# Performance work log

Measured on AMD Instinct MI355X. Metric: run time of the kernel, lower is better.

## Reference

```python
import jax, jax.numpy as jnp
import numpy as np

MAX_CAV = 5


def setup_inputs() -> dict:
    key = jax.random.key(0)
    k1, k2, k3, k4, k5 = jax.random.split(key, 5)
    # ragged group lengths, each <= MAX_CAV, sum = 25
    record_len = jnp.array([3, 5, 2, 4, 1, 5, 3, 2], dtype=jnp.int32)
    N, C, H, W = 25, 256, 48, 176
    x = jax.random.normal(k1, (N, C, H, W), dtype=jnp.float32)
    W1 = jax.random.normal(k2, (MAX_CAV, 2 * MAX_CAV), dtype=jnp.float32) * 0.3
    W2 = jax.random.normal(k3, (MAX_CAV, MAX_CAV), dtype=jnp.float32) * 0.3
    conv_w = jax.random.normal(k4, (MAX_CAV,), dtype=jnp.float32) * 0.3
    conv_b = jax.random.normal(k5, (1,), dtype=jnp.float32) * 0.1
    return dict(x=x, record_len=record_len, W1=W1, W2=W2, conv_w=conv_w, conv_b=conv_b)


def _pad_regroup(x, record_len, max_cav):
    # scatter ragged tokens into a zero-padded [bs, max_cav, C, H, W] buffer
    N = x.shape[0]
    bs = record_len.shape[0]
    cum = jnp.cumsum(record_len)
    tok = jnp.arange(N)
    b = jnp.searchsorted(cum, tok, side='right')      # batch id per token
    slot = tok - (cum[b] - record_len[b])             # position within group
    padded = jnp.zeros((bs, max_cav) + x.shape[1:], x.dtype)
    return padded.at[b, slot].set(x)


def reference(x, record_len, W1, W2, conv_w, conv_b):
    padded = _pad_regroup(x, record_len, MAX_CAV)     # [bs, M, C, H, W]
    # AdaptiveAvg/MaxPool3d(1) over (C,H,W); padded slots are all-zero -> max=0
    x_avg = padded.mean(axis=(2, 3, 4))               # [bs, M]
    x_max = padded.max(axis=(2, 3, 4))                # [bs, M]
    x_sq = jnp.concatenate([x_avg, x_max], axis=1)    # [bs, 2M]
    gate = jax.nn.relu(jax.nn.sigmoid(x_sq @ W1.T) @ W2.T)  # [bs, M]
    scaled = padded * gate[:, :, None, None, None]
    # 1x1x1 Conv3d(M -> 1) == weighted sum over CAV axis + bias, then ReLU
    out = jax.nn.relu(jnp.einsum('m,bmchw->bchw', conv_w, scaled) + conv_b[0])
    return out
```

## Files before the change

### kernel.cpp

```cpp
#include <hip/hip_runtime.h>
#include <hip/hip_bf16.h>
#include <math.h>

#define CHW      2162688
#define V4       540672
#define BPT      64
#define V4_BLK   8448
#define ITERS    33
#define MAXCAV   5

typedef float f32x4 __attribute__((ext_vector_type(4)));

__global__ __launch_bounds__(256) void k_reduce(const float4* __restrict__ x,
                                                float* __restrict__ psum,
                                                float* __restrict__ pmax) {
    const int t   = blockIdx.y;
    const int blk = blockIdx.x;
    const long base = (long)t * V4 + (long)blk * V4_BLK;

    float s = 0.0f;
    float mx = -INFINITY;
    #pragma unroll 4
    for (int i = 0; i < ITERS; ++i) {
        float4 v = x[base + i * 256 + threadIdx.x];
        s += (v.x + v.y) + (v.z + v.w);
        mx = fmaxf(mx, fmaxf(fmaxf(v.x, v.y), fmaxf(v.z, v.w)));
    }

    __shared__ float ssum[256];
    __shared__ float smax[256];
    ssum[threadIdx.x] = s;
    smax[threadIdx.x] = mx;
    __syncthreads();
    #pragma unroll
    for (int off = 128; off > 0; off >>= 1) {
        if (threadIdx.x < off) {
            ssum[threadIdx.x] += ssum[threadIdx.x + off];
            smax[threadIdx.x] = fmaxf(smax[threadIdx.x], smax[threadIdx.x + off]);
        }
        __syncthreads();
    }
    if (threadIdx.x == 0) {
        psum[t * BPT + blk] = ssum[0];
        pmax[t * BPT + blk] = smax[0];
    }
}

__global__ __launch_bounds__(256) void k_gate(const float* __restrict__ psum,
                                              const float* __restrict__ pmax,
                                              const int*   __restrict__ record_len,
                                              const float* __restrict__ W1,
                                              const float* __restrict__ W2,
                                              const float* __restrict__ conv_w,
                                              int*   __restrict__ starts,
                                              float* __restrict__ coefs,
                                              int bs, int ntok) {
    __shared__ float tsum[32];
    __shared__ float tmax[32];
    const int wave = threadIdx.x >> 6;
    const int lane = threadIdx.x & 63;

    for (int t = wave; t < ntok; t += 4) {
        float s = psum[t * BPT + lane];
        float m = pmax[t * BPT + lane];
        #pragma unroll
        for (int off = 32; off > 0; off >>= 1) {
            s += __shfl_xor(s, off, 64);
            m = fmaxf(m, __shfl_xor(m, off, 64));
        }
        if (lane == 0) { tsum[t] = s; tmax[t] = m; }
    }
    __syncthreads();

    if ((int)threadIdx.x < bs) {
        const int b = threadIdx.x;
        int start = 0;
        for (int i = 0; i < b; ++i) start += record_len[i];
        const int len = record_len[b];

        float xsq[2 * MAXCAV];
        #pragma unroll
        for (int m = 0; m < MAXCAV; ++m) {
            const bool valid = m < len;
            xsq[m]          = valid ? tsum[start + m] * (1.0f / (float)CHW) : 0.0f;
            xsq[MAXCAV + m] = valid ? tmax[start + m] : 0.0f;
        }
        float h[MAXCAV];
        #pragma unroll
        for (int j = 0; j < MAXCAV; ++j) {
            float a = 0.0f;
            #pragma unroll
            for (int k = 0; k < 2 * MAXCAV; ++k) a += xsq[k] * W1[j * 2 * MAXCAV + k];
            h[j] = 1.0f / (1.0f + expf(-a));
        }
        starts[b] = start;
        #pragma unroll
        for (int m = 0; m < MAXCAV; ++m) {
            float g = 0.0f;
            #pragma unroll
            for (int j = 0; j < MAXCAV; ++j) g += h[j] * W2[m * MAXCAV + j];
            g = fmaxf(g, 0.0f);
            coefs[b * MAXCAV + m] = conv_w[m] * g;
        }
    }
}

template <int LEN>
__device__ __forceinline__ void apply_one(const float4* __restrict__ x,
                                          const float* __restrict__ c,
                                          float bias, int start,
                                          long obase, int idx,
                                          float4* __restrict__ out) {
    float ax = bias, ay = bias, az = bias, aw = bias;
    #pragma unroll
    for (int m = 0; m < LEN; ++m) {
        float4 v = x[(long)(start + m) * V4 + idx];
        ax += c[m] * v.x;
        ay += c[m] * v.y;
        az += c[m] * v.z;
        aw += c[m] * v.w;
    }
    f32x4 acc;
    acc.x = fmaxf(ax, 0.0f);
    acc.y = fmaxf(ay, 0.0f);
    acc.z = fmaxf(az, 0.0f);
    acc.w = fmaxf(aw, 0.0f);
    __builtin_nontemporal_store(acc, (f32x4*)(out + obase + idx));
}

template <int LEN>
__device__ __forceinline__ void apply_pair(const float4* __restrict__ x,
                                           const float* __restrict__ c,
                                           float bias, int start,
                                           long obase, int idx0,
                                           float4* __restrict__ out) {
    apply_one<LEN>(x, c, bias, start, obase, idx0, out);
    apply_one<LEN>(x, c, bias, start, obase, idx0 + 256, out);
}

__global__ __launch_bounds__(256) void k_apply(const float4* __restrict__ x,
                                               const int*   __restrict__ record_len,
                                               const int*   __restrict__ starts,
                                               const float* __restrict__ coefs,
                                               const float* __restrict__ conv_b,
                                               float4* __restrict__ out,
                                               int bs) {
    const int idx0 = blockIdx.x * 512 + threadIdx.x;
    const float bias = conv_b[0];

    for (int b = 0; b < bs; ++b) {
        const int len   = record_len[b];
        const int start = starts[b];
        float c[MAXCAV];
        #pragma unroll
        for (int m = 0; m < MAXCAV; ++m) c[m] = coefs[b * MAXCAV + m];
        const long obase = (long)b * V4;

        switch (len) {
            case 1:  apply_pair<1>(x, c, bias, start, obase, idx0, out); break;
            case 2:  apply_pair<2>(x, c, bias, start, obase, idx0, out); break;
            case 3:  apply_pair<3>(x, c, bias, start, obase, idx0, out); break;
            case 4:  apply_pair<4>(x, c, bias, start, obase, idx0, out); break;
            default: apply_pair<5>(x, c, bias, start, obase, idx0, out); break;
        }
    }
}

extern "C" void kernel_launch(void* const* d_in, const int* in_sizes, int n_in,
                              void* d_out, int out_size, void* d_ws, size_t ws_size,
                              hipStream_t stream) {
    const float* x  = (const float*)d_in[0];
    const int*   rl = (const int*)d_in[1];
    const float* W1 = (const float*)d_in[2];
    const float* W2 = (const float*)d_in[3];
    const float* cw = (const float*)d_in[4];
    const float* cb = (const float*)d_in[5];
    float4* out = (float4*)d_out;

    char* ws = (char*)d_ws;
    float* psum   = (float*)(ws);
    float* pmax   = (float*)(ws + 6400);
    int*   starts = (int*)  (ws + 12800);
    float* coefs  = (float*)(ws + 12832);

    const int ntok = in_sizes[0] / CHW;
    const int bs   = in_sizes[1];

    k_reduce<<<dim3(BPT, ntok), 256, 0, stream>>>((const float4*)x, psum, pmax);
    k_gate<<<1, 256, 0, stream>>>(psum, pmax, rl, W1, W2, cw, starts, coefs, bs, ntok);
    k_apply<<<V4 / 512, 256, 0, stream>>>((const float4*)x, rl, starts, coefs, cb, out, bs);
}
```

Before: 84.66 us.

## Fuse reduce, gate and apply into one cooperative persistent kernel

Replaces the three-kernel pipeline with a single cooperative kernel of 1024 blocks. Each block first reduces a contiguous chunk of x that may straddle two tokens, then a grid-wide sync follows, every block recomputes the gate coefficients redundantly, and then applies the weighted sum to its slice. This is meant to remove two kernel launch gaps and the serial single-block gate kernel, at the cost of a grid barrier and repeated gate work in every block. It keeps the old three-kernel path as a fallback when occupancy is too low.

```diff
diff --git a/kernel.cpp b/kernel.cpp
--- a/kernel.cpp
+++ b/kernel.cpp
@@ -1,15 +1,186 @@
 #include <hip/hip_runtime.h>
-#include <hip/hip_bf16.h>
+#include <hip/hip_cooperative_groups.h>
 #include <math.h>
 
-#define CHW      2162688
-#define V4       540672
+#define CHW     2162688
+#define V4      540672
+#define NTOK    25
+#define NBLK    1024
+#define CHUNK1  13200
+#define CHUNK3  528
+#define MAXCAV  5
+#define NBATCH  8
+
 #define BPT      64
 #define V4_BLK   8448
 #define ITERS    33
-#define MAXCAV   5
-
+
+namespace cg = cooperative_groups;
 typedef float f32x4 __attribute__((ext_vector_type(4)));
+
+__device__ __forceinline__ void relu_store(float ax, float ay, float az, float aw,
+                                           float4* __restrict__ out, int o) {
+    f32x4 acc;
+    acc.x = fmaxf(ax, 0.0f);
+    acc.y = fmaxf(ay, 0.0f);
+    acc.z = fmaxf(az, 0.0f);
+    acc.w = fmaxf(aw, 0.0f);
+    __builtin_nontemporal_store(acc, (f32x4*)(out + o));
+}
+
+template <int LEN>
+__device__ __forceinline__ void apply_idx(const float4* __restrict__ x,
+                                          const float* c, float bias,
+                                          int start, int obase, int idx,
+                                          float4* __restrict__ out) {
+    float ax = bias, ay = bias, az = bias, aw = bias;
+    #pragma unroll
+    for (int m = 0; m < LEN; ++m) {
+        float4 v = x[(start + m) * V4 + idx];
+        ax += c[m] * v.x;
+        ay += c[m] * v.y;
+        az += c[m] * v.z;
+        aw += c[m] * v.w;
+    }
+    relu_store(ax, ay, az, aw, out, obase + idx);
+}
+
+template <int LEN>
+__device__ __forceinline__ void apply_chunk(const float4* __restrict__ x,
+                                            const float* c, float bias,
+                                            int start, int obase, int base3,
+                                            int tid, float4* __restrict__ out) {
+    apply_idx<LEN>(x, c, bias, start, obase, base3 + tid, out);
+    apply_idx<LEN>(x, c, bias, start, obase, base3 + 256 + tid, out);
+    if (tid < CHUNK3 - 512)
+        apply_idx<LEN>(x, c, bias, start, obase, base3 + 512 + tid, out);
+}
+
+__global__ __launch_bounds__(256, 4) void k_fused(
+    const float4* __restrict__ x,
+    const int*   __restrict__ record_len,
+    const float* __restrict__ W1,
+    const float* __restrict__ W2,
+    const float* __restrict__ conv_w,
+    const float* __restrict__ conv_b,
+    float4* __restrict__ out,
+    float* __restrict__ ps,
+    float* __restrict__ pm)
+{
+    const int tid  = threadIdx.x;
+    const int bid  = blockIdx.x;
+    const int lane = tid & 63;
+    const int wave = tid >> 6;
+
+    const int base  = bid * CHUNK1;
+    const int t0    = base / V4;
+    const int split = min((t0 + 1) * V4 - base, CHUNK1);
+
+    float s0 = 0.f, s1 = 0.f, m0 = -INFINITY, m1 = -INFINITY;
+    #pragma unroll 2
+    for (int li = tid; li < CHUNK1; li += 256) {
+        float4 v = x[base + li];
+        float vs = (v.x + v.y) + (v.z + v.w);
+        float vm = fmaxf(fmaxf(v.x, v.y), fmaxf(v.z, v.w));
+        if (li < split) { s0 += vs; m0 = fmaxf(m0, vm); }
+        else            { s1 += vs; m1 = fmaxf(m1, vm); }
+    }
+    #pragma unroll
+    for (int off = 32; off > 0; off >>= 1) {
+        s0 += __shfl_xor(s0, off, 64);
+        s1 += __shfl_xor(s1, off, 64);
+        m0 = fmaxf(m0, __shfl_xor(m0, off, 64));
+        m1 = fmaxf(m1, __shfl_xor(m1, off, 64));
+    }
+    __shared__ float rs0[4], rs1[4], rm0[4], rm1[4];
+    if (lane == 0) { rs0[wave] = s0; rs1[wave] = s1; rm0[wave] = m0; rm1[wave] = m1; }
+    __syncthreads();
+    if (tid == 0) {
+        ps[2 * bid]     = rs0[0] + rs0[1] + rs0[2] + rs0[3];
+        ps[2 * bid + 1] = rs1[0] + rs1[1] + rs1[2] + rs1[3];
+        pm[2 * bid]     = fmaxf(fmaxf(rm0[0], rm0[1]), fmaxf(rm0[2], rm0[3]));
+        pm[2 * bid + 1] = fmaxf(fmaxf(rm1[0], rm1[1]), fmaxf(rm1[2], rm1[3]));
+    }
+
+    cg::this_grid().sync();
+
+    __shared__ float tsum[NTOK], tmax[NTOK];
+    __shared__ float scoef[NBATCH][MAXCAV];
+    __shared__ int   sstart[NBATCH], slen[NBATCH];
+    __shared__ float sbias;
+
+    for (int t = wave; t < NTOK; t += 4) {
+        const int b_lo = (t == 0) ? 0 : ((t - 1) * V4 + CHUNK1 - 1) / CHUNK1;
+        const int b_hi = min(NBLK - 1, ((t + 1) * V4 + CHUNK1 - 1) / CHUNK1 - 1);
+        float s = 0.f, m = -INFINITY;
+        for (int b = b_lo + lane; b <= b_hi; b += 64) {
+            const int tb = (b * CHUNK1) / V4;
+            if (tb == t)     { s += ps[2 * b];     m = fmaxf(m, pm[2 * b]); }
+            if (tb == t - 1) { s += ps[2 * b + 1]; m = fmaxf(m, pm[2 * b + 1]); }
+        }
+        #pragma unroll
+        for (int off = 32; off > 0; off >>= 1) {
+            s += __shfl_xor(s, off, 64);
+            m = fmaxf(m, __shfl_xor(m, off, 64));
+        }
+        if (lane == 0) { tsum[t] = s; tmax[t] = m; }
+    }
+    __syncthreads();
+
+    if (tid < NBATCH) {
+        const int b = tid;
+        int start = 0;
+        for (int i = 0; i < b; ++i) start += record_len[i];
+        const int len = record_len[b];
+        sstart[b] = start;
+        slen[b]   = len;
+
+        float xsq[2 * MAXCAV];
+        #pragma unroll
+        for (int m = 0; m < MAXCAV; ++m) {
+            const bool valid = m < len;
+            xsq[m]          = valid ? tsum[start + m] * (1.0f / (float)CHW) : 0.0f;
+            xsq[MAXCAV + m] = valid ? tmax[start + m] : 0.0f;
+        }
+        float h[MAXCAV];
+        #pragma unroll
+        for (int j = 0; j < MAXCAV; ++j) {
+            float a = 0.0f;
+            #pragma unroll
+            for (int k = 0; k < 2 * MAXCAV; ++k) a += xsq[k] * W1[j * 2 * MAXCAV + k];
+            h[j] = 1.0f / (1.0f + expf(-a));
+        }
+        #pragma unroll
+        for (int m = 0; m < MAXCAV; ++m) {
+            float g = 0.0f;
+            #pragma unroll
+            for (int j = 0; j < MAXCAV; ++j) g += h[j] * W2[m * MAXCAV + j];
+            scoef[b][m] = conv_w[m] * fmaxf(g, 0.0f);
+        }
+        if (b == 0) sbias = conv_b[0];
+    }
+    __syncthreads();
+
+    const float bias  = sbias;
+    const int   base3 = bid * CHUNK3;
+
+    for (int b = 0; b < NBATCH; ++b) {
+        const int len   = slen[b];
+        const int start = sstart[b];
+        float c[MAXCAV];
+        #pragma unroll
+        for (int m = 0; m < MAXCAV; ++m) c[m] = scoef[b][m];
+        const int obase = b * V4;
+
+        switch (len) {
+            case 1:  apply_chunk<1>(x, c, bias, start, obase, base3, tid, out); break;
+            case 2:  apply_chunk<2>(x, c, bias, start, obase, base3, tid, out); break;
+            case 3:  apply_chunk<3>(x, c, bias, start, obase, base3, tid, out); break;
+            case 4:  apply_chunk<4>(x, c, bias, start, obase, base3, tid, out); break;
+            default: apply_chunk<5>(x, c, bias, start, obase, base3, tid, out); break;
+        }
+    }
+}
 
 __global__ __launch_bounds__(256) void k_reduce(const float4* __restrict__ x,
                                                 float* __restrict__ psum,
@@ -99,43 +270,18 @@
             float g = 0.0f;
             #pragma unroll
             for (int j = 0; j < MAXCAV; ++j) g += h[j] * W2[m * MAXCAV + j];
-            g = fmaxf(g, 0.0f);
-            coefs[b * MAXCAV + m] = conv_w[m] * g;
+            coefs[b * MAXCAV + m] = conv_w[m] * fmaxf(g, 0.0f);
         }
     }
 }
 
 template <int LEN>
-__device__ __forceinline__ void apply_one(const float4* __restrict__ x,
-                                          const float* __restrict__ c,
-                                          float bias, int start,
-                                          long obase, int idx,
-                                          float4* __restrict__ out) {
-    float ax = bias, ay = bias, az = bias, aw = bias;
-    #pragma unroll
-    for (int m = 0; m < LEN; ++m) {
-        float4 v = x[(long)(start + m) * V4 + idx];
-        ax += c[m] * v.x;
-        ay += c[m] * v.y;
-        az += c[m] * v.z;
-        aw += c[m] * v.w;
-    }
-    f32x4 acc;
-    acc.x = fmaxf(ax, 0.0f);
-    acc.y = fmaxf(ay, 0.0f);
-    acc.z = fmaxf(az, 0.0f);
-    acc.w = fmaxf(aw, 0.0f);
-    __builtin_nontemporal_store(acc, (f32x4*)(out + obase + idx));
-}
-
-template <int LEN>
-__device__ __forceinline__ void apply_pair(const float4* __restrict__ x,
-                                           const float* __restrict__ c,
-                                           float bias, int start,
-                                           long obase, int idx0,
-                                           float4* __restrict__ out) {
-    apply_one<LEN>(x, c, bias, start, obase, idx0, out);
-    apply_one<LEN>(x, c, bias, start, obase, idx0 + 256, out);
+__device__ __forceinline__ void fb_pair(const float4* __restrict__ x,
+                                        const float* c, float bias, int start,
+                                        long obase, int idx0,
+                                        float4* __restrict__ out) {
+    apply_idx<LEN>(x, c, bias, start, (int)obase, idx0, out);
+    apply_idx<LEN>(x, c, bias, start, (int)obase, idx0 + 256, out);
 }
 
 __global__ __launch_bounds__(256) void k_apply(const float4* __restrict__ x,
@@ -157,11 +303,11 @@
         const long obase = (long)b * V4;
 
         switch (len) {
-            case 1:  apply_pair<1>(x, c, bias, start, obase, idx0, out); break;
-            case 2:  apply_pair<2>(x, c, bias, start, obase, idx0, out); break;
-            case 3:  apply_pair<3>(x, c, bias, start, obase, idx0, out); break;
-            case 4:  apply_pair<4>(x, c, bias, start, obase, idx0, out); break;
-            default: apply_pair<5>(x, c, bias, start, obase, idx0, out); break;
+            case 1:  fb_pair<1>(x, c, bias, start, obase, idx0, out); break;
+            case 2:  fb_pair<2>(x, c, bias, start, obase, idx0, out); break;
+            case 3:  fb_pair<3>(x, c, bias, start, obase, idx0, out); break;
+            case 4:  fb_pair<4>(x, c, bias, start, obase, idx0, out); break;
+            default: fb_pair<5>(x, c, bias, start, obase, idx0, out); break;
         }
     }
 }
@@ -169,24 +315,36 @@
 extern "C" void kernel_launch(void* const* d_in, const int* in_sizes, int n_in,
                               void* d_out, int out_size, void* d_ws, size_t ws_size,
                               hipStream_t stream) {
-    const float* x  = (const float*)d_in[0];
-    const int*   rl = (const int*)d_in[1];
-    const float* W1 = (const float*)d_in[2];
-    const float* W2 = (const float*)d_in[3];
-    const float* cw = (const float*)d_in[4];
-    const float* cb = (const float*)d_in[5];
+    const float4* x  = (const float4*)d_in[0];
+    const int*    rl = (const int*)d_in[1];
+    const float*  W1 = (const float*)d_in[2];
+    const float*  W2 = (const float*)d_in[3];
+    const float*  cw = (const float*)d_in[4];
+    const float*  cb = (const float*)d_in[5];
     float4* out = (float4*)d_out;
 
     char* ws = (char*)d_ws;
-    float* psum   = (float*)(ws);
-    float* pmax   = (float*)(ws + 6400);
-    int*   starts = (int*)  (ws + 12800);
-    float* coefs  = (float*)(ws + 12832);
+    float* ps     = (float*)(ws);
+    float* pm     = (float*)(ws + 8192);
+    float* psum   = (float*)(ws + 16384);
+    float* pmax   = (float*)(ws + 16384 + 6400);
+    int*   starts = (int*)  (ws + 16384 + 12800);
+    float* coefs  = (float*)(ws + 16384 + 12832);
 
     const int ntok = in_sizes[0] / CHW;
     const int bs   = in_sizes[1];
 
-    k_reduce<<<dim3(BPT, ntok), 256, 0, stream>>>((const float4*)x, psum, pmax);
-    k_gate<<<1, 256, 0, stream>>>(psum, pmax, rl, W1, W2, cw, starts, coefs, bs, ntok);
-    k_apply<<<V4 / 512, 256, 0, stream>>>((const float4*)x, rl, starts, coefs, cb, out, bs);
-}
+    int occ = 0;
+    hipOccupancyMaxActiveBlocksPerMultiprocessor(&occ, k_fused, 256, 0);
+
+    if (occ >= 4) {
+        void* args[] = { (void*)&x, (void*)&rl, (void*)&W1, (void*)&W2,
+                         (void*)&cw, (void*)&cb, (void*)&out, (void*)&ps, (void*)&pm };
+        hipLaunchCooperativeKernel((void*)k_fused, dim3(NBLK), dim3(256),
+                                   args, 0, stream);
+    } else {
+        k_reduce<<<dim3(BPT, ntok), 256, 0, stream>>>(x, psum, pmax);
+        k_gate<<<1, 256, 0, stream>>>(psum, pmax, rl, W1, W2, cw, starts, coefs, bs, ntok);
+        k_apply<<<V4 / 512, 256, 0, stream>>>(x, rl, starts, coefs, cb, out, bs);
+    }
+}
```

Result: slower. 189.0 us (+123.2%).
